# Performance work log

Hardware: AMD Instinct MI355X
Metric: run time of the kernel (lower is better)

Reference implementation:

```python
import jax, jax.numpy as jnp
import numpy as np

B, L, H = 32, 512, 1024
H2 = H // 2          # split half = 512
D_ATTN = 64
EPS = 1e-5


def setup_inputs() -> dict:
    key = jax.random.key(0)
    ks = jax.random.split(key, 6)
    x = jax.random.normal(ks[0], (B, L, H), dtype=jnp.float32)
    # LayerNorm params (default torch init: weight=1, bias=0)
    ln_gamma = jnp.ones((H2,), jnp.float32)
    ln_beta = jnp.zeros((H2,), jnp.float32)
    # Toeplitz params (module inits w_vector=0, bias=1; use small random w for nontrivial math)
    w_vector = jax.random.normal(ks[1], (2 * L - 1,), jnp.float32) * 0.02
    t_bias = jnp.ones((L,), jnp.float32)
    # TinyAttention: kqv Linear(H2 -> 3*d_attn), proj Linear(d_attn -> H2)
    kqv_w = jax.random.normal(ks[2], (H2, 3 * D_ATTN), jnp.float32) * 0.02
    kqv_b = jnp.zeros((3 * D_ATTN,), jnp.float32)
    proj_w = jax.random.normal(ks[3], (D_ATTN, H2), jnp.float32) * 0.02
    proj_b = jnp.zeros((H2,), jnp.float32)
    return {"x": x, "ln_gamma": ln_gamma, "ln_beta": ln_beta,
            "w_vector": w_vector, "t_bias": t_bias,
            "kqv_w": kqv_w, "kqv_b": kqv_b, "proj_w": proj_w, "proj_b": proj_b}


def _toeplitz(w_vector):
    # Faithful replication of get_toeplitz(): pad, tile, trim, reshape, crop.
    r = w_vector.shape[0] // 2            # = L - 1
    t = jnp.pad(w_vector, (0, L))         # length 3L - 1
    t = jnp.tile(t, L)[:-L]               # length L * (3L - 2)
    t = t.reshape(L, 3 * L - 2)
    return t[:, r:-r]                      # [L, L]


def _tiny_attention(v, kqv_w, kqv_b, proj_w, proj_b):
    kqv = v @ kqv_w + kqv_b                        # [B, L, 3*d_attn]
    k, q, val = jnp.split(kqv, 3, axis=-1)         # chunk order: key, query, value
    scale = 1.0 / jnp.sqrt(jnp.float32(q.shape[-1]))
    scores = jnp.einsum('bqd,bkd->bqk', q, k) * scale
    soft = jax.nn.softmax(scores, axis=-1)
    head = jnp.einsum('bqk,bkd->bqd', soft, val)   # [B, L, d_attn]
    return head @ proj_w + proj_b                  # [B, L, H2]


def reference(x, ln_gamma, ln_beta, w_vector, t_bias, kqv_w, kqv_b, proj_w, proj_b):
    u, v = jnp.split(x, 2, axis=-1)                # each [B, L, H2]
    head = _tiny_attention(v, kqv_w, kqv_b, proj_w, proj_b)
    # LayerNorm over last dim
    mu = jnp.mean(v, axis=-1, keepdims=True)
    var = jnp.mean(jnp.square(v - mu), axis=-1, keepdims=True)
    vn = (v - mu) * jax.lax.rsqrt(var + EPS) * ln_gamma + ln_beta
    # spatial (Toeplitz) mixing: permute -> [B, H2, L], matmul [L, L], bias
    w_t = _toeplitz(w_vector)
    vm = jnp.einsum('blc,lm->bmc', vn, w_t.T).transpose(0, 2, 1)  # keep faithful: vp @ w_t
    vm = jnp.einsum('bcl,lm->bcm', vn.transpose(0, 2, 1), w_t) + t_bias
    v_out = vm.transpose(0, 2, 1) + head           # [B, L, H2]
    return u * v_out
```

## Files before the change

### kernel.cpp

```cpp
#include <hip/hip_runtime.h>
#include <math.h>

#define NB 32
#define LL 512
#define HH 1024
#define H2 512
#define DA 64

typedef unsigned int u32;
typedef unsigned short u16;
typedef __bf16 bf16x8 __attribute__((ext_vector_type(8)));
typedef float f32x4 __attribute__((ext_vector_type(4)));
typedef u16 u16x8 __attribute__((ext_vector_type(8)));

__device__ __forceinline__ u16 f2bu(float f) {
    u32 u = __builtin_bit_cast(u32, f);
    u = (u + 0x7fff + ((u >> 16) & 1)) >> 16;
    return (u16)u;
}

__device__ __forceinline__ float b2f(u16 u) {
    u32 v = (u32)u << 16;
    return __builtin_bit_cast(float, v);
}

__device__ __forceinline__ void async_cp16(const void* g, void* l) {
    __builtin_amdgcn_global_load_lds(
        (const __attribute__((address_space(1))) u32*)g,
        (__attribute__((address_space(3))) u32*)l, 16, 0, 0);
}

__global__ void prep_kernel(const float* __restrict__ wv,
                            const float* __restrict__ kqvw,
                            const float* __restrict__ projw,
                            u16* __restrict__ wt, u16* __restrict__ kqvwT,
                            u16* __restrict__ projwT) {
    int e = blockIdx.x * 256 + threadIdx.x;
    if (e < 262144) {
        int m = e >> 9, l = e & 511;
        wt[e] = f2bu(wv[511 + m - l]);
    } else if (e < 262144 + 98304) {
        int i = e - 262144;
        int n = i >> 9, k = i & 511;
        kqvwT[i] = f2bu(kqvw[(size_t)k * 192 + n]);
    } else {
        int i = e - 360448;
        int c = i >> 6, d = i & 63;
        projwT[i] = f2bu(projw[(size_t)d * 512 + c]);
    }
}

__global__ __launch_bounds__(256, 1)
void v_kernel(const float* __restrict__ x,
              const u16* __restrict__ kqvwT, const float* __restrict__ kqvb,
              const float* __restrict__ gamma, const float* __restrict__ beta,
              u16* __restrict__ vnT,
              u16* __restrict__ qb, u16* __restrict__ kb, u16* __restrict__ vT) {
    __shared__ u16 Af[64 * 64 * 8];
    __shared__ u16 Bs_[2][192 * 64];
    __shared__ float MU[64], RS[64];
    int blk = blockIdx.x, t = threadIdx.x;
    int R0 = blk * 64, b = R0 >> 9, l0 = R0 & 511;
    int lane = t & 63, wid = t >> 6;
    int l15 = lane & 15, q16 = lane >> 4, q8 = q16 * 8;
    int wm = (wid & 1) * 32, wn = (wid >> 1) * 96;
    const float* xg = x + (size_t)R0 * HH + H2;

    int arow[4], af4[4], sgg[4], shalf[4];
#pragma unroll
    for (int p = 0; p < 4; ++p) {
        int flat = t + p * 256;
        arow[p] = flat >> 4; af4[p] = flat & 15;
        sgg[p] = (af4[p] >> 1) ^ (arow[p] & 7);
        shalf[p] = (af4[p] & 1) * 4;
    }

    float s1[4] = {0.f, 0.f, 0.f, 0.f}, s2[4] = {0.f, 0.f, 0.f, 0.f};
    float4 av[4];
    f32x4 acc[2][6] = {};

#pragma unroll
    for (int s = 0; s < 6; ++s) {
        int ci = t + s * 256;
        int grow = ci >> 3, gcol = ((ci & 7) ^ (grow & 7)) << 3;
        async_cp16(kqvwT + (size_t)grow * 512 + gcol, &Bs_[0][ci * 8]);
    }
#pragma unroll
    for (int p = 0; p < 4; ++p)
        av[p] = *(const float4*)(xg + (size_t)arow[p] * HH + af4[p] * 4);
#pragma unroll
    for (int p = 0; p < 4; ++p) {
        s1[p] += av[p].x + av[p].y + av[p].z + av[p].w;
        s2[p] += av[p].x * av[p].x + av[p].y * av[p].y
               + av[p].z * av[p].z + av[p].w * av[p].w;
        ushort4 pk;
        pk.x = f2bu(av[p].x); pk.y = f2bu(av[p].y);
        pk.z = f2bu(av[p].z); pk.w = f2bu(av[p].w);
        *(ushort4*)(&Af[(arow[p] * 64 + sgg[p]) * 8 + shalf[p]]) = pk;
    }
    __syncthreads();

    for (int it = 0; it < 8; ++it) {
        int nx = it + 1, nb = nx & 1, cb = it & 1;
        if (it < 7) {
            int k0n = nx * 64;
#pragma unroll
            for (int p = 0; p < 4; ++p)
                av[p] = *(const float4*)(xg + (size_t)arow[p] * HH + k0n + af4[p] * 4);
#pragma unroll
            for (int s = 0; s < 6; ++s) {
                int ci = t + s * 256;
                int grow = ci >> 3, gcol = ((ci & 7) ^ (grow & 7)) << 3;
                async_cp16(kqvwT + (size_t)grow * 512 + k0n + gcol, &Bs_[nb][ci * 8]);
            }
        }
        const u16* Bp = &Bs_[cb][0];
#pragma unroll
        for (int kk = 0; kk < 2; ++kk) {
            int j0 = kk * 4 + q16;
            int g = it * 8 + kk * 4 + q16;
            bf16x8 a[2];
#pragma unroll
            for (int i = 0; i < 2; ++i) {
                int row = wm + i * 16 + l15;
                a[i] = *(const bf16x8*)(&Af[(row * 64 + (g ^ (row & 7))) * 8]);
            }
#pragma unroll
            for (int j = 0; j < 6; ++j) {
                int n = wn + j * 16 + l15;
                bf16x8 bb = *(const bf16x8*)(Bp + (n * 8 + (j0 ^ (n & 7))) * 8);
#pragma unroll
                for (int i = 0; i < 2; ++i)
                    acc[i][j] = __builtin_amdgcn_mfma_f32_16x16x32_bf16(a[i], bb, acc[i][j], 0, 0, 0);
            }
        }
        if (it < 7) {
            int k0n = nx * 64;
#pragma unroll
            for (int p = 0; p < 4; ++p) {
                s1[p] += av[p].x + av[p].y + av[p].z + av[p].w;
                s2[p] += av[p].x * av[p].x + av[p].y * av[p].y
                       + av[p].z * av[p].z + av[p].w * av[p].w;
                ushort4 pk;
                pk.x = f2bu(av[p].x); pk.y = f2bu(av[p].y);
                pk.z = f2bu(av[p].z); pk.w = f2bu(av[p].w);
                *(ushort4*)(&Af[(arow[p] * 64 + nx * 8 + sgg[p]) * 8 + shalf[p]]) = pk;
            }
        }
        __syncthreads();
    }

#pragma unroll
    for (int p = 0; p < 4; ++p) {
        s1[p] += __shfl_xor(s1[p], 1); s2[p] += __shfl_xor(s2[p], 1);
        s1[p] += __shfl_xor(s1[p], 2); s2[p] += __shfl_xor(s2[p], 2);
        s1[p] += __shfl_xor(s1[p], 4); s2[p] += __shfl_xor(s2[p], 4);
        s1[p] += __shfl_xor(s1[p], 8); s2[p] += __shfl_xor(s2[p], 8);
    }
    if ((t & 15) == 0) {
        int g = t >> 4;
#pragma unroll
        for (int p = 0; p < 4; ++p) {
            float mu = s1[p] * (1.0f / H2);
            float rstd = rsqrtf(s2[p] * (1.0f / H2) - mu * mu + 1e-5f);
            MU[p * 16 + g] = mu; RS[p * 16 + g] = rstd;
        }
    }

    u16* Ks = &Bs_[0][0];
    u16* Qs = &Bs_[0][4096];
    u16* Vs = &Bs_[1][0];
    int rq = q16 * 4;
#pragma unroll
    for (int i = 0; i < 2; ++i) {
#pragma unroll
        for (int j = 0; j < 6; ++j) {
            int n = wn + j * 16 + l15;
            float bias = kqvb[n];
#pragma unroll
            for (int rr = 0; rr < 4; ++rr) {
                int m = wm + i * 16 + rq + rr;
                u16 hv = f2bu(acc[i][j][rr] + bias);
                if (n < 64)       Ks[m * 64 + n] = hv;
                else if (n < 128) Qs[m * 64 + (n - 64)] = hv;
                else              Vs[(n - 128) * 72 + m] = hv;
            }
        }
    }
    __syncthreads();
    {
        size_t base = (size_t)R0 * 64 + t * 16;
        *(uint4*)(kb + base)     = *(const uint4*)(Ks + t * 16);
        *(uint4*)(kb + base + 8) = *(const uint4*)(Ks + t * 16 + 8);
        *(uint4*)(qb + base)     = *(const uint4*)(Qs + t * 16);
        *(uint4*)(qb + base + 8) = *(const uint4*)(Qs + t * 16 + 8);
        int d = t >> 2, ls = (t & 3) * 16;
        u16* vd = vT + ((size_t)(b * 64 + d)) * 512 + l0 + ls;
        *(uint4*)(vd)     = *(const uint4*)(Vs + d * 72 + ls);
        *(uint4*)(vd + 8) = *(const uint4*)(Vs + d * 72 + ls + 8);
    }

    {
        int c0 = 2 * t;
        float ga0 = gamma[c0], ga1 = gamma[c0 + 1];
        float be0 = beta[c0],  be1 = beta[c0 + 1];
        u16* d0 = vnT + ((size_t)(b * H2 + c0)) * LL + l0;
        u16* d1 = d0 + LL;
        int gbase = t >> 2;
        int coff = c0 & 7;
#pragma unroll
        for (int lc = 0; lc < 8; ++lc) {
            u16x8 o0, o1;
#pragma unroll
            for (int li = 0; li < 8; ++li) {
                int l = lc * 8 + li;
                u32 w = *(const u32*)(&Af[(l * 64 + (gbase ^ (l & 7))) * 8 + coff]);
                float mu = MU[l], rs = RS[l];
                o0[li] = f2bu((b2f((u16)w)         - mu) * rs * ga0 + be0);
                o1[li] = f2bu((b2f((u16)(w >> 16)) - mu) * rs * ga1 + be1);
            }
            *(u16x8*)(d0 + lc * 8) = o0;
            *(u16x8*)(d1 + lc * 8) = o1;
        }
    }
}

#define VLD 136
__global__ __launch_bounds__(256, 4)
void attn_kernel(const u16* __restrict__ qb, const u16* __restrict__ kb,
                 const u16* __restrict__ vT, u16* __restrict__ head) {
    __shared__ u16 Ps[4 * 16 * VLD];
    __shared__ float Osh[4][16 * 65];
    __shared__ float Msh[4][16], Lsh[4][16];
    int b = blockIdx.y, q0 = blockIdx.x * 16;
    int t = threadIdx.x, lane = t & 63, w = t >> 6;
    int l15 = lane & 15, q16 = lane >> 4, q8 = q16 * 8;
    int kc = w * 128;
    const u16* qg = qb + (size_t)b * LL * DA;
    const u16* kg = kb + (size_t)b * LL * DA;
    const u16* vg = vT + (size_t)b * DA * LL;

    bf16x8 aq[2];
#pragma unroll
    for (int s = 0; s < 2; ++s)
        aq[s] = *(const bf16x8*)(qg + (size_t)(q0 + l15) * DA + s * 32 + q8);

    f32x4 sc[8] = {};
#pragma unroll
    for (int j = 0; j < 8; ++j) {
#pragma unroll
        for (int s = 0; s < 2; ++s) {
            bf16x8 bk = *(const bf16x8*)(kg + (size_t)(kc + j * 16 + l15) * DA + s * 32 + q8);
            sc[j] = __builtin_amdgcn_mfma_f32_16x16x32_bf16(aq[s], bk, sc[j], 0, 0, 0);
        }
    }
    float mx[4], sm[4];
#pragma unroll
    for (int j = 0; j < 8; ++j)
#pragma unroll
        for (int rr = 0; rr < 4; ++rr) sc[j][rr] *= 0.125f;
#pragma unroll
    for (int rr = 0; rr < 4; ++rr) {
        float m0 = sc[0][rr];
#pragma unroll
        for (int j = 1; j < 8; ++j) m0 = fmaxf(m0, sc[j][rr]);
        m0 = fmaxf(m0, __shfl_xor(m0, 1));
        m0 = fmaxf(m0, __shfl_xor(m0, 2));
        m0 = fmaxf(m0, __shfl_xor(m0, 4));
        m0 = fmaxf(m0, __shfl_xor(m0, 8));
        mx[rr] = m0;
    }
#pragma unroll
    for (int j = 0; j < 8; ++j)
#pragma unroll
        for (int rr = 0; rr < 4; ++rr) sc[j][rr] = __expf(sc[j][rr] - mx[rr]);
#pragma unroll
    for (int rr = 0; rr < 4; ++rr) {
        float s0 = sc[0][rr];
#pragma unroll
        for (int j = 1; j < 8; ++j) s0 += sc[j][rr];
        s0 += __shfl_xor(s0, 1);
        s0 += __shfl_xor(s0, 2);
        s0 += __shfl_xor(s0, 4);
        s0 += __shfl_xor(s0, 8);
        sm[rr] = s0;
    }
    u16* Pw = Ps + w * 16 * VLD;
#pragma unroll
    for (int j = 0; j < 8; ++j)
#pragma unroll
        for (int rr = 0; rr < 4; ++rr)
            Pw[(q16 * 4 + rr) * VLD + j * 16 + l15] = f2bu(sc[j][rr]);
    f32x4 o[4] = {};
#pragma unroll
    for (int kt = 0; kt < 4; ++kt) {
        bf16x8 ap = *(const bf16x8*)(Pw + l15 * VLD + kt * 32 + q8);
#pragma unroll
        for (int j = 0; j < 4; ++j) {
            bf16x8 bv = *(const bf16x8*)(vg + (size_t)(j * 16 + l15) * LL + kc + kt * 32 + q8);
            o[j] = __builtin_amdgcn_mfma_f32_16x16x32_bf16(ap, bv, o[j], 0, 0, 0);
        }
    }
#pragma unroll
    for (int j = 0; j < 4; ++j)
#pragma unroll
        for (int rr = 0; rr < 4; ++rr)
            Osh[w][(q16 * 4 + rr) * 65 + j * 16 + l15] = o[j][rr];
    if (l15 == 0) {
#pragma unroll
        for (int rr = 0; rr < 4; ++rr) {
            Msh[w][q16 * 4 + rr] = mx[rr];
            Lsh[w][q16 * 4 + rr] = sm[rr];
        }
    }
    __syncthreads();
    int qq = t >> 4, dg = (t & 15) * 4;
    float m0 = Msh[0][qq], m1 = Msh[1][qq], m2 = Msh[2][qq], m3 = Msh[3][qq];
    float ms = fmaxf(fmaxf(m0, m1), fmaxf(m2, m3));
    float f0 = __expf(m0 - ms), f1 = __expf(m1 - ms), f2 = __expf(m2 - ms), f3 = __expf(m3 - ms);
    float lst = Lsh[0][qq] * f0 + Lsh[1][qq] * f1 + Lsh[2][qq] * f2 + Lsh[3][qq] * f3;
    float inv = 1.0f / lst;
    ushort4 res;
    u16* rp = (u16*)&res;
#pragma unroll
    for (int i = 0; i < 4; ++i) {
        int idx = qq * 65 + dg + i;
        float a = Osh[0][idx] * f0 + Osh[1][idx] * f1 + Osh[2][idx] * f2 + Osh[3][idx] * f3;
        rp[i] = f2bu(a * inv);
    }
    *(ushort4*)(head + (size_t)(b * LL + q0 + qq) * DA + dg) = res;
}

__device__ __forceinline__ void mfma_tile64(const u16* As, const u16* Bs,
                                            f32x4 acc[4][4], int wm, int wn,
                                            int l15, int q16) {
    int s7 = l15 & 7;
#pragma unroll
    for (int kk = 0; kk < 2; ++kk) {
        int j0 = kk * 4 + q16;
        bf16x8 a[4], bv[4];
#pragma unroll
        for (int i = 0; i < 4; ++i) {
            int row = wm + i * 16 + l15;
            a[i] = *(const bf16x8*)(As + (row * 8 + (j0 ^ s7)) * 8);
        }
#pragma unroll
        for (int j = 0; j < 4; ++j) {
            int row = wn + j * 16 + l15;
            bv[j] = *(const bf16x8*)(Bs + (row * 8 + (j0 ^ s7)) * 8);
        }
#pragma unroll
        for (int i = 0; i < 4; ++i)
#pragma unroll
            for (int j = 0; j < 4; ++j)
                acc[i][j] = __builtin_amdgcn_mfma_f32_16x16x32_bf16(a[i], bv[j], acc[i][j], 0, 0, 0);
    }
}

__device__ __forceinline__ void stage_pair(const u16* A, const u16* B, int ldk,
                                           int koff, u16* Ad, u16* Bd, int t) {
#pragma unroll
    for (int s = 0; s < 4; ++s) {
        int ci = t + s * 256;
        int grow = ci >> 3, gcol = ((ci & 7) ^ (grow & 7)) << 3;
        async_cp16(A + (size_t)grow * ldk + koff + gcol, Ad + ci * 8);
        async_cp16(B + (size_t)grow * ldk + koff + gcol, Bd + ci * 8);
    }
}

__global__ __launch_bounds__(256, 2)
void mix_kernel(const u16* __restrict__ wt,
                const u16* __restrict__ vnT,
                const u16* __restrict__ headb,
                const u16* __restrict__ projwT,
                const float* __restrict__ x,
                const float* __restrict__ tbias,
                const float* __restrict__ projb,
                float* __restrict__ out) {
    __shared__ u16 As[2][128 * 64];
    __shared__ u16 Bs[2][128 * 64];
    int lid = blockIdx.x;
    int p8 = lid & 7, rest = lid >> 3;
    int mi = rest & 3, pair = (rest >> 2) * 8 + p8;
    int b = pair >> 2, m0 = mi * 128, c0 = (pair & 3) * 128;
    int t = threadIdx.x, lane = t & 63, wid = t >> 6;
    int wm = (wid >> 1) * 64, wn = (wid & 1) * 64;
    int l15 = lane & 15, q16 = lane >> 4;
    f32x4 acc[4][4] = {};
    const u16* Ag = wt + (size_t)m0 * 512;
    const u16* Bg = vnT + ((size_t)b * H2 + c0) * 512;
    const u16* Hg = headb + ((size_t)b * LL + m0) * DA;
    const u16* Pg = projwT + (size_t)c0 * DA;

    stage_pair(Ag, Bg, 512, 0, As[0], Bs[0], t);
    __syncthreads();

    for (int it = 0; it < 9; ++it) {
        int nx = it + 1;
        if (nx < 8)
            stage_pair(Ag, Bg, 512, nx * 64, As[nx & 1], Bs[nx & 1], t);
        else if (nx == 8)
            stage_pair(Hg, Pg, 64, 0, As[0], Bs[0], t);
        mfma_tile64(As[it & 1], Bs[it & 1], acc, wm, wn, l15, q16);
        __syncthreads();
    }

    int rq = q16 * 4;
#pragma unroll
    for (int i = 0; i < 4; ++i) {
#pragma unroll
        for (int rr = 0; rr < 4; ++rr) {
            int m = m0 + wm + i * 16 + rq + rr;
            float tb = tbias[m];
            const float* xrow = x + ((size_t)b * LL + m) * HH;
            float* orow = out + ((size_t)b * LL + m) * H2;
#pragma unroll
            for (int j = 0; j < 4; ++j) {
                int c = c0 + wn + j * 16 + l15;
                float val = acc[i][j][rr] + tb + projb[c];
                orow[c] = xrow[c] * val;
            }
        }
    }
}

extern "C" void kernel_launch(void* const* d_in, const int* in_sizes, int n_in,
                              void* d_out, int out_size, void* d_ws, size_t ws_size,
                              hipStream_t stream) {
    (void)in_sizes; (void)n_in; (void)out_size; (void)ws_size;
    const float* x     = (const float*)d_in[0];
    const float* gamma = (const float*)d_in[1];
    const float* beta  = (const float*)d_in[2];
    const float* wv    = (const float*)d_in[3];
    const float* tb    = (const float*)d_in[4];
    const float* kqvw  = (const float*)d_in[5];
    const float* kqvb  = (const float*)d_in[6];
    const float* projw = (const float*)d_in[7];
    const float* projb = (const float*)d_in[8];
    float* out = (float*)d_out;

    u16* vnT_bf  = (u16*)d_ws;
    u16* qb      = vnT_bf + (size_t)NB * LL * H2;
    u16* kb      = qb + (size_t)NB * LL * DA;
    u16* vTb     = kb + (size_t)NB * LL * DA;
    u16* head_bf = vTb + (size_t)NB * LL * DA;
    u16* wt_bf   = head_bf + (size_t)NB * LL * DA;
    u16* kqvwT   = wt_bf + 512 * 512;
    u16* projwT  = kqvwT + 192 * 512;

    prep_kernel <<<1536, 256, 0, stream>>>(wv, kqvw, projw, wt_bf, kqvwT, projwT);
    v_kernel    <<<256, 256, 0, stream>>>(x, kqvwT, kqvb, gamma, beta,
                                          vnT_bf, qb, kb, vTb);
    attn_kernel <<<dim3(32, NB), 256, 0, stream>>>(qb, kb, vTb, head_bf);
    mix_kernel  <<<512, 256, 0, stream>>>(wt_bf, vnT_bf, head_bf, projwT,
                                          x, tb, projb, out);
}
```

Baseline: 173.6 us.

## Widen v_kernel to 512 threads and stage mix epilogue through LDS

v_kernel now runs 512 threads per block with eight waves, each owning a 16-row slice, so per-thread loads, MFMAs and LayerNorm output work are halved. This aims for more latency hiding over only 256 blocks. mix_kernel's epilogue now writes the accumulators to shared memory, then reads back contiguous float4 rows so the x loads and output stores are coalesced and vectorized, instead of scattered scalar accesses. The cost is an extra LDS round trip and barrier, plus lower per-thread ILP in v_kernel.

```diff
diff --git a/kernel.cpp b/kernel.cpp
--- a/kernel.cpp
+++ b/kernel.cpp
@@ -50,7 +50,7 @@
     }
 }
 
-__global__ __launch_bounds__(256, 1)
+__global__ __launch_bounds__(512, 1)
 void v_kernel(const float* __restrict__ x,
               const u16* __restrict__ kqvwT, const float* __restrict__ kqvb,
               const float* __restrict__ gamma, const float* __restrict__ beta,
@@ -63,33 +63,33 @@
     int R0 = blk * 64, b = R0 >> 9, l0 = R0 & 511;
     int lane = t & 63, wid = t >> 6;
     int l15 = lane & 15, q16 = lane >> 4, q8 = q16 * 8;
-    int wm = (wid & 1) * 32, wn = (wid >> 1) * 96;
+    int wm = (wid & 3) * 16, wn = (wid >> 2) * 96;
     const float* xg = x + (size_t)R0 * HH + H2;
 
-    int arow[4], af4[4], sgg[4], shalf[4];
-#pragma unroll
-    for (int p = 0; p < 4; ++p) {
-        int flat = t + p * 256;
+    int arow[2], af4[2], sgg[2], shalf[2];
+#pragma unroll
+    for (int p = 0; p < 2; ++p) {
+        int flat = t + p * 512;
         arow[p] = flat >> 4; af4[p] = flat & 15;
         sgg[p] = (af4[p] >> 1) ^ (arow[p] & 7);
         shalf[p] = (af4[p] & 1) * 4;
     }
 
-    float s1[4] = {0.f, 0.f, 0.f, 0.f}, s2[4] = {0.f, 0.f, 0.f, 0.f};
-    float4 av[4];
-    f32x4 acc[2][6] = {};
-
-#pragma unroll
-    for (int s = 0; s < 6; ++s) {
-        int ci = t + s * 256;
+    float s1[2] = {0.f, 0.f}, s2[2] = {0.f, 0.f};
+    float4 av[2];
+    f32x4 acc[6] = {};
+
+#pragma unroll
+    for (int s = 0; s < 3; ++s) {
+        int ci = t + s * 512;
         int grow = ci >> 3, gcol = ((ci & 7) ^ (grow & 7)) << 3;
         async_cp16(kqvwT + (size_t)grow * 512 + gcol, &Bs_[0][ci * 8]);
     }
 #pragma unroll
-    for (int p = 0; p < 4; ++p)
+    for (int p = 0; p < 2; ++p)
         av[p] = *(const float4*)(xg + (size_t)arow[p] * HH + af4[p] * 4);
 #pragma unroll
-    for (int p = 0; p < 4; ++p) {
+    for (int p = 0; p < 2; ++p) {
         s1[p] += av[p].x + av[p].y + av[p].z + av[p].w;
         s2[p] += av[p].x * av[p].x + av[p].y * av[p].y
                + av[p].z * av[p].z + av[p].w * av[p].w;
@@ -105,11 +105,11 @@
         if (it < 7) {
             int k0n = nx * 64;
 #pragma unroll
-            for (int p = 0; p < 4; ++p)
+            for (int p = 0; p < 2; ++p)
                 av[p] = *(const float4*)(xg + (size_t)arow[p] * HH + k0n + af4[p] * 4);
 #pragma unroll
-            for (int s = 0; s < 6; ++s) {
-                int ci = t + s * 256;
+            for (int s = 0; s < 3; ++s) {
+                int ci = t + s * 512;
                 int grow = ci >> 3, gcol = ((ci & 7) ^ (grow & 7)) << 3;
                 async_cp16(kqvwT + (size_t)grow * 512 + k0n + gcol, &Bs_[nb][ci * 8]);
             }
@@ -119,25 +119,18 @@
         for (int kk = 0; kk < 2; ++kk) {
             int j0 = kk * 4 + q16;
             int g = it * 8 + kk * 4 + q16;
-            bf16x8 a[2];
-#pragma unroll
-            for (int i = 0; i < 2; ++i) {
-                int row = wm + i * 16 + l15;
-                a[i] = *(const bf16x8*)(&Af[(row * 64 + (g ^ (row & 7))) * 8]);
-            }
+            int row = wm + l15;
+            bf16x8 a = *(const bf16x8*)(&Af[(row * 64 + (g ^ (row & 7))) * 8]);
 #pragma unroll
             for (int j = 0; j < 6; ++j) {
                 int n = wn + j * 16 + l15;
                 bf16x8 bb = *(const bf16x8*)(Bp + (n * 8 + (j0 ^ (n & 7))) * 8);
-#pragma unroll
-                for (int i = 0; i < 2; ++i)
-                    acc[i][j] = __builtin_amdgcn_mfma_f32_16x16x32_bf16(a[i], bb, acc[i][j], 0, 0, 0);
+                acc[j] = __builtin_amdgcn_mfma_f32_16x16x32_bf16(a, bb, acc[j], 0, 0, 0);
             }
         }
         if (it < 7) {
-            int k0n = nx * 64;
-#pragma unroll
-            for (int p = 0; p < 4; ++p) {
+#pragma unroll
+            for (int p = 0; p < 2; ++p) {
                 s1[p] += av[p].x + av[p].y + av[p].z + av[p].w;
                 s2[p] += av[p].x * av[p].x + av[p].y * av[p].y
                        + av[p].z * av[p].z + av[p].w * av[p].w;
@@ -151,19 +144,18 @@
     }
 
 #pragma unroll
-    for (int p = 0; p < 4; ++p) {
+    for (int p = 0; p < 2; ++p) {
         s1[p] += __shfl_xor(s1[p], 1); s2[p] += __shfl_xor(s2[p], 1);
         s1[p] += __shfl_xor(s1[p], 2); s2[p] += __shfl_xor(s2[p], 2);
         s1[p] += __shfl_xor(s1[p], 4); s2[p] += __shfl_xor(s2[p], 4);
         s1[p] += __shfl_xor(s1[p], 8); s2[p] += __shfl_xor(s2[p], 8);
     }
     if ((t & 15) == 0) {
-        int g = t >> 4;
-#pragma unroll
-        for (int p = 0; p < 4; ++p) {
+#pragma unroll
+        for (int p = 0; p < 2; ++p) {
             float mu = s1[p] * (1.0f / H2);
             float rstd = rsqrtf(s2[p] * (1.0f / H2) - mu * mu + 1e-5f);
-            MU[p * 16 + g] = mu; RS[p * 16 + g] = rstd;
+            MU[arow[p]] = mu; RS[arow[p]] = rstd;
         }
     }
 
@@ -172,55 +164,43 @@
     u16* Vs = &Bs_[1][0];
     int rq = q16 * 4;
 #pragma unroll
-    for (int i = 0; i < 2; ++i) {
-#pragma unroll
-        for (int j = 0; j < 6; ++j) {
-            int n = wn + j * 16 + l15;
-            float bias = kqvb[n];
-#pragma unroll
-            for (int rr = 0; rr < 4; ++rr) {
-                int m = wm + i * 16 + rq + rr;
-                u16 hv = f2bu(acc[i][j][rr] + bias);
-                if (n < 64)       Ks[m * 64 + n] = hv;
-                else if (n < 128) Qs[m * 64 + (n - 64)] = hv;
-                else              Vs[(n - 128) * 72 + m] = hv;
-            }
+    for (int j = 0; j < 6; ++j) {
+        int n = wn + j * 16 + l15;
+        float bias = kqvb[n];
+#pragma unroll
+        for (int rr = 0; rr < 4; ++rr) {
+            int m = wm + rq + rr;
+            u16 hv = f2bu(acc[j][rr] + bias);
+            if (n < 64)       Ks[m * 64 + n] = hv;
+            else if (n < 128) Qs[m * 64 + (n - 64)] = hv;
+            else              Vs[(n - 128) * 72 + m] = hv;
         }
     }
     __syncthreads();
     {
-        size_t base = (size_t)R0 * 64 + t * 16;
-        *(uint4*)(kb + base)     = *(const uint4*)(Ks + t * 16);
-        *(uint4*)(kb + base + 8) = *(const uint4*)(Ks + t * 16 + 8);
-        *(uint4*)(qb + base)     = *(const uint4*)(Qs + t * 16);
-        *(uint4*)(qb + base + 8) = *(const uint4*)(Qs + t * 16 + 8);
-        int d = t >> 2, ls = (t & 3) * 16;
+        size_t base = (size_t)R0 * 64 + t * 8;
+        *(uint4*)(kb + base) = *(const uint4*)(Ks + t * 8);
+        *(uint4*)(qb + base) = *(const uint4*)(Qs + t * 8);
+        int d = t >> 3, ls = (t & 7) * 8;
         u16* vd = vT + ((size_t)(b * 64 + d)) * 512 + l0 + ls;
-        *(uint4*)(vd)     = *(const uint4*)(Vs + d * 72 + ls);
-        *(uint4*)(vd + 8) = *(const uint4*)(Vs + d * 72 + ls + 8);
+        *(uint4*)(vd) = *(const uint4*)(Vs + d * 72 + ls);
     }
 
     {
-        int c0 = 2 * t;
-        float ga0 = gamma[c0], ga1 = gamma[c0 + 1];
-        float be0 = beta[c0],  be1 = beta[c0 + 1];
-        u16* d0 = vnT + ((size_t)(b * H2 + c0)) * LL + l0;
-        u16* d1 = d0 + LL;
-        int gbase = t >> 2;
-        int coff = c0 & 7;
+        int c = t;
+        float ga = gamma[c], be = beta[c];
+        u16* d0 = vnT + ((size_t)(b * H2 + c)) * LL + l0;
+        int gbase = c >> 3, coff = c & 7;
 #pragma unroll
         for (int lc = 0; lc < 8; ++lc) {
-            u16x8 o0, o1;
+            u16x8 o0;
 #pragma unroll
             for (int li = 0; li < 8; ++li) {
                 int l = lc * 8 + li;
-                u32 w = *(const u32*)(&Af[(l * 64 + (gbase ^ (l & 7))) * 8 + coff]);
-                float mu = MU[l], rs = RS[l];
-                o0[li] = f2bu((b2f((u16)w)         - mu) * rs * ga0 + be0);
-                o1[li] = f2bu((b2f((u16)(w >> 16)) - mu) * rs * ga1 + be1);
+                u16 w = Af[(l * 64 + (gbase ^ (l & 7))) * 8 + coff];
+                o0[li] = f2bu((b2f(w) - MU[l]) * RS[l] * ga + be);
             }
             *(u16x8*)(d0 + lc * 8) = o0;
-            *(u16x8*)(d1 + lc * 8) = o1;
         }
     }
 }
@@ -377,8 +357,9 @@
                 const float* __restrict__ tbias,
                 const float* __restrict__ projb,
                 float* __restrict__ out) {
-    __shared__ u16 As[2][128 * 64];
-    __shared__ u16 Bs[2][128 * 64];
+    __shared__ u16 SMEM[4][128 * 64];
+    u16* As0 = SMEM[0]; u16* As1 = SMEM[1];
+    u16* Bs0 = SMEM[2]; u16* Bs1 = SMEM[3];
     int lid = blockIdx.x;
     int p8 = lid & 7, rest = lid >> 3;
     int mi = rest & 3, pair = (rest >> 2) * 8 + p8;
@@ -392,34 +373,47 @@
     const u16* Hg = headb + ((size_t)b * LL + m0) * DA;
     const u16* Pg = projwT + (size_t)c0 * DA;
 
-    stage_pair(Ag, Bg, 512, 0, As[0], Bs[0], t);
+    stage_pair(Ag, Bg, 512, 0, As0, Bs0, t);
     __syncthreads();
 
     for (int it = 0; it < 9; ++it) {
         int nx = it + 1;
         if (nx < 8)
-            stage_pair(Ag, Bg, 512, nx * 64, As[nx & 1], Bs[nx & 1], t);
+            stage_pair(Ag, Bg, 512, nx * 64, (nx & 1) ? As1 : As0,
+                       (nx & 1) ? Bs1 : Bs0, t);
         else if (nx == 8)
-            stage_pair(Hg, Pg, 64, 0, As[0], Bs[0], t);
-        mfma_tile64(As[it & 1], Bs[it & 1], acc, wm, wn, l15, q16);
+            stage_pair(Hg, Pg, 64, 0, As0, Bs0, t);
+        mfma_tile64((it & 1) ? As1 : As0, (it & 1) ? Bs1 : Bs0,
+                    acc, wm, wn, l15, q16);
         __syncthreads();
     }
 
+    float* Acc = (float*)&SMEM[0][0];
     int rq = q16 * 4;
 #pragma unroll
-    for (int i = 0; i < 4; ++i) {
-#pragma unroll
-        for (int rr = 0; rr < 4; ++rr) {
-            int m = m0 + wm + i * 16 + rq + rr;
+    for (int i = 0; i < 4; ++i)
+#pragma unroll
+        for (int j = 0; j < 4; ++j)
+#pragma unroll
+            for (int rr = 0; rr < 4; ++rr)
+                Acc[(wm + i * 16 + rq + rr) * 128 + (wn + j * 16 + l15)] = acc[i][j][rr];
+    __syncthreads();
+    {
+        int cq = (t & 31) * 4, rg = (t >> 5) * 16;
+        float4 pj = *(const float4*)(projb + c0 + cq);
+#pragma unroll
+        for (int rr3 = 0; rr3 < 16; ++rr3) {
+            int mrow = rg + rr3;
+            int m = m0 + mrow;
             float tb = tbias[m];
-            const float* xrow = x + ((size_t)b * LL + m) * HH;
-            float* orow = out + ((size_t)b * LL + m) * H2;
-#pragma unroll
-            for (int j = 0; j < 4; ++j) {
-                int c = c0 + wn + j * 16 + l15;
-                float val = acc[i][j][rr] + tb + projb[c];
-                orow[c] = xrow[c] * val;
-            }
+            float4 a4 = *(const float4*)(Acc + mrow * 128 + cq);
+            float4 xv = *(const float4*)(x + ((size_t)b * LL + m) * HH + c0 + cq);
+            float4 o;
+            o.x = xv.x * (a4.x + tb + pj.x);
+            o.y = xv.y * (a4.y + tb + pj.y);
+            o.z = xv.z * (a4.z + tb + pj.z);
+            o.w = xv.w * (a4.w + tb + pj.w);
+            *(float4*)(out + ((size_t)b * LL + m) * H2 + c0 + cq) = o;
         }
     }
 }
@@ -449,7 +443,7 @@
     u16* projwT  = kqvwT + 192 * 512;
 
     prep_kernel <<<1536, 256, 0, stream>>>(wv, kqvw, projw, wt_bf, kqvwT, projwT);
-    v_kernel    <<<256, 256, 0, stream>>>(x, kqvwT, kqvb, gamma, beta,
+    v_kernel    <<<256, 512, 0, stream>>>(x, kqvwT, kqvb, gamma, beta,
                                           vnT_bf, qb, kb, vTb);
     attn_kernel <<<dim3(32, NB), 256, 0, stream>>>(qb, kb, vTb, head_bf);
     mix_kernel  <<<512, 256, 0, stream>>>(wt_bf, vnT_bf, head_bf, projwT,
```

Result: faster. 163.5 us (-5.8%).
